# Kernel tuning notes

Measured on AMD Instinct MI355X. Metric: run time of the kernel, lower is better.

Reference implementation:

```python
import jax, jax.numpy as jnp
import numpy as np

B, D, H, O, E, K = 8192, 1024, 4096, 1024, 8, 2

def setup_inputs() -> dict:
    key = jax.random.key(0)
    ks = jax.random.split(key, 8)
    x = jax.random.normal(ks[0], (B, D), dtype=jnp.float32)
    topk_idx = jax.random.randint(ks[1], (B, K), 0, E, dtype=jnp.int32)
    weights = jax.random.uniform(ks[2], (B, K), dtype=jnp.float32)
    s1 = 1.0 / np.sqrt(D)
    s2 = 1.0 / np.sqrt(H)
    W1 = jax.random.uniform(ks[3], (E, D, H), minval=-s1, maxval=s1, dtype=jnp.float32)
    b1 = jax.random.uniform(ks[4], (E, H), minval=-s1, maxval=s1, dtype=jnp.float32)
    W2 = jax.random.uniform(ks[5], (E, H, O), minval=-s2, maxval=s2, dtype=jnp.float32)
    b2 = jax.random.uniform(ks[6], (E, O), minval=-s2, maxval=s2, dtype=jnp.float32)
    return {"x": x, "topk_idx": topk_idx, "weights": weights,
            "W1": W1, "b1": b1, "W2": W2, "b2": b2}

def reference(x, topk_idx, weights, W1, b1, W2, b2):
    # Per-token gate mass for each expert: gate[b,e] = sum_i weights[b,i]*[topk_idx[b,i]==e]
    # Equivalent to the original masked gather/scatter combine (duplicates in topk_idx sum).
    out = jnp.zeros((x.shape[0], W2.shape[-1]), dtype=x.dtype)
    for e in range(W1.shape[0]):  # small fixed loop over experts
        gate_e = jnp.sum(weights * (topk_idx == e), axis=1)  # [B]
        h = jax.nn.relu(x @ W1[e] + b1[e])                   # [B,H]
        out_e = h @ W2[e] + b2[e]                            # [B,O]
        out = out + gate_e[:, None] * out_e
    return out
```

## Files before the change

### kernel.cpp

```cpp
#include <hip/hip_runtime.h>
#include <stdint.h>

#define B_TOK 8192
#define D_DIM 1024
#define H_DIM 4096
#define O_DIM 1024
#define E_NUM 8
#define K_TOP 2
#define NPAIR (B_TOK * K_TOP)

typedef short bf16x8 __attribute__((ext_vector_type(8)));
typedef float f32x4 __attribute__((ext_vector_type(4)));

struct Hdr {
    int counts[8];
    int offsets[9];
    int total1, total2;
    int base1[9];
    int base2[9];
};

__device__ __forceinline__ unsigned short f2bf(float f) {
    union { float f; unsigned int u; } v; v.f = f;
    unsigned int u = v.u;
    unsigned int r = (u + 0x7fffu + ((u >> 16) & 1u)) >> 16;
    return (unsigned short)r;
}

__device__ __forceinline__ float bf2f(unsigned short s) {
    union { unsigned int u; float f; } v;
    v.u = ((unsigned int)s) << 16;
    return v.f;
}

__device__ __forceinline__ void async16(const void* g, const void* l) {
    __builtin_amdgcn_global_load_lds(
        (__attribute__((address_space(1))) void*)(uintptr_t)g,
        (__attribute__((address_space(3))) void*)(uint32_t)(uintptr_t)l,
        16, 0, 0);
}


__global__ void cvt_x_kernel(const float* __restrict__ x, unsigned short* __restrict__ xb) {
    int i = (blockIdx.x * 256 + threadIdx.x) * 4;
    float4 v = *(const float4*)(x + i);
    ushort4 o;
    o.x = f2bf(v.x); o.y = f2bf(v.y); o.z = f2bf(v.z); o.w = f2bf(v.w);
    *(ushort4*)(xb + i) = o;
}

__global__ __launch_bounds__(256) void tconv2_kernel(const float* __restrict__ W1,
                                                     const float* __restrict__ W2,
                                                     unsigned short* __restrict__ o1,
                                                     unsigned short* __restrict__ o2) {
    __shared__ unsigned short tb[64 * 134];
    int z = blockIdx.y;
    int bid = blockIdx.x;
    int R, C;
    const float* ip;
    unsigned short* op;
    if (z < 8) {
        R = D_DIM; C = H_DIM;
        ip = W1 + (size_t)z * R * C;
        op = o1 + (size_t)z * R * C;
    } else {
        R = H_DIM; C = O_DIM;
        ip = W2 + (size_t)(z - 8) * R * C;
        op = o2 + (size_t)(z - 8) * R * C;
    }
    int tR = R >> 7;
    int r0 = (bid % tR) * 128;
    int c0 = (bid / tR) * 64;
    int tid = threadIdx.x;

    int rl = tid >> 4;
    int cg = (tid & 15) * 4;
#pragma unroll
    for (int p = 0; p < 8; p++) {
        int r = rl + p * 16;
        float4 v = *(const float4*)&ip[(size_t)(r0 + r) * C + c0 + cg];
        tb[(cg + 0) * 134 + r] = f2bf(v.x);
        tb[(cg + 1) * 134 + r] = f2bf(v.y);
        tb[(cg + 2) * 134 + r] = f2bf(v.z);
        tb[(cg + 3) * 134 + r] = f2bf(v.w);
    }
    __syncthreads();

    int r16 = (tid & 15) * 8;
#pragma unroll
    for (int i = 0; i < 4; i++) {
        int c = (tid >> 4) + i * 16;
        uint4 v = *(const uint4*)&tb[c * 134 + r16];
        *(uint4*)&op[(size_t)(c0 + c) * R + r0 + r16] = v;
    }
}


__global__ __launch_bounds__(1024) void route_kernel(const int* __restrict__ topk,
                                                     Hdr* hdr,
                                                     int* __restrict__ ptok,
                                                     int* __restrict__ pslot) {
    __shared__ int wcnt[16][8];
    __shared__ int wcur[16][8];
    int tid = threadIdx.x;
    int w = tid >> 6;
    if ((tid & 63) < 8) wcnt[w][tid & 63] = 0;
    __syncthreads();
    int ev[16];
#pragma unroll
    for (int j = 0; j < 16; j++) {
        ev[j] = topk[tid + j * 1024];
        atomicAdd(&wcnt[w][ev[j]], 1);
    }
    __syncthreads();
    if (tid == 0) {
        int off = 0, t1 = 0, t2 = 0;
        for (int e = 0; e < 8; e++) {
            int c = 0;
            for (int w2 = 0; w2 < 16; w2++) {
                wcur[w2][e] = off + c;
                c += wcnt[w2][e];
            }
            hdr->counts[e] = c;
            hdr->offsets[e] = off;
            hdr->base1[e] = t1;
            hdr->base2[e] = t2;
            t1 += ((c + 255) >> 8) * (H_DIM / 256);
            t2 += ((c + 127) >> 7) * (O_DIM / 128);
            off += c;
        }
        hdr->offsets[8] = off;
        hdr->base1[8] = t1;
        hdr->base2[8] = t2;
        hdr->total1 = t1;
        hdr->total2 = t2;
    }
    __syncthreads();
#pragma unroll
    for (int j = 0; j < 16; j++) {
        int i = tid + j * 1024;
        int pos = atomicAdd(&wcur[w][ev[j]], 1);
        ptok[pos] = i >> 1;
        pslot[i] = pos;
    }
}

__global__ void ws_fail_kernel(float* out) { out[0] = 1.0e9f; }


#define ASL(BUF, KH) ((BUF) * 32768 + (KH) * 16384)

#define STG_A(BUF, KH, KOFF) do { \
    async16(Ab + srcA[0] + (KOFF), smem + ASL(BUF, KH) + wu * 2048); \
    async16(Ab + srcA[1] + (KOFF), smem + ASL(BUF, KH) + wu * 2048 + 1024); } while (0)

#define STG_B(BUF, KH, KOFF) do { \
    async16(Bb + srcB[0] + (KOFF), smem + 65536 + ASL(BUF, KH) + wu * 2048); \
    async16(Bb + srcB[1] + (KOFF), smem + 65536 + ASL(BUF, KH) + wu * 2048 + 1024); } while (0)

#define VM6 asm volatile("s_waitcnt vmcnt(6)" ::: "memory")
#define VM0 asm volatile("s_waitcnt vmcnt(0)" ::: "memory")
#define NOPX ((void)0)

#define PHASE0(BUF, KH, STAGE, CKPT) do { \
    STAGE; \
    bq[0] = *(const bf16x8*)&smem[pBo[0] + ASL(BUF, KH)]; \
    bq[1] = *(const bf16x8*)&smem[pBo[1] + ASL(BUF, KH)]; \
    bq[2] = *(const bf16x8*)&smem[pBo[2] + ASL(BUF, KH)]; \
    bq[3] = *(const bf16x8*)&smem[pBo[3] + ASL(BUF, KH)]; \
    aq[0] = *(const bf16x8*)&smem[pAo[0] + ASL(BUF, KH)]; \
    aq[1] = *(const bf16x8*)&smem[pAo[1] + ASL(BUF, KH)]; \
    aq[2] = *(const bf16x8*)&smem[pAo[2] + ASL(BUF, KH)]; \
    aq[3] = *(const bf16x8*)&smem[pAo[3] + ASL(BUF, KH)]; \
    __builtin_amdgcn_s_barrier(); \
    asm volatile("s_waitcnt lgkmcnt(0)" ::: "memory"); \
    __builtin_amdgcn_s_setprio(1); \
    _Pragma("unroll") \
    for (int q_ = 0; q_ < 4; ++q_) { \
        _Pragma("unroll") \
        for (int n_ = 0; n_ < 4; ++n_) \
            acc[q_][n_] = __builtin_amdgcn_mfma_f32_16x16x32_bf16(aq[q_], bq[n_], acc[q_][n_], 0, 0, 0); \
    } \
    __builtin_amdgcn_s_setprio(0); \
    CKPT; \
    __builtin_amdgcn_s_barrier(); \
} while (0)

#define PHASE1(BUF, KH, STAGE, CKPT) do { \
    STAGE; \
    aq[0] = *(const bf16x8*)&smem[pAo[4] + ASL(BUF, KH)]; \
    aq[1] = *(const bf16x8*)&smem[pAo[5] + ASL(BUF, KH)]; \
    aq[2] = *(const bf16x8*)&smem[pAo[6] + ASL(BUF, KH)]; \
    aq[3] = *(const bf16x8*)&smem[pAo[7] + ASL(BUF, KH)]; \
    __builtin_amdgcn_s_barrier(); \
    asm volatile("s_waitcnt lgkmcnt(0)" ::: "memory"); \
    __builtin_amdgcn_s_setprio(1); \
    _Pragma("unroll") \
    for (int q_ = 0; q_ < 4; ++q_) { \
        _Pragma("unroll") \
        for (int n_ = 0; n_ < 4; ++n_) \
            acc[4 + q_][n_] = __builtin_amdgcn_mfma_f32_16x16x32_bf16(aq[q_], bq[n_], acc[4 + q_][n_], 0, 0, 0); \
    } \
    __builtin_amdgcn_s_setprio(0); \
    CKPT; \
    __builtin_amdgcn_s_barrier(); \
} while (0)

template <int KD, int N, bool GATHER>
__global__ __launch_bounds__(512, 2) void moe_gemm256_kernel(
    const unsigned short* __restrict__ A,
    const unsigned short* __restrict__ Bt,
    const float* __restrict__ bias,
    const Hdr* __restrict__ hdr,
    const int* __restrict__ ptok,
    unsigned short* __restrict__ outp,
    int phase) {

    extern __shared__ __align__(16) char smem[];
    constexpr int NT = KD / 64;
    constexpr int NI = NT / 2;
    static_assert(NT >= 4 && (NT % 2) == 0, "K-tile count");

    const int tid = threadIdx.x;
    const int lane = tid & 63;
    const int wv = tid >> 6;
    const int wu = __builtin_amdgcn_readfirstlane(wv);
    const int lr = lane & 15;
    const int lkg = lane >> 4;
    const int wr = wv >> 2;
    const int wc = wv & 3;

    const int total = hdr->total1;
    const int* tb = hdr->base1;

    int chunk = (total + 7) >> 3;
    int seq = (blockIdx.x & 7) * chunk + (blockIdx.x >> 3);
    if (seq >= total) return;

    int e = 0;
#pragma unroll
    for (int j = 1; j < 8; j++)
        if (seq >= tb[j]) e = j;
    e = __builtin_amdgcn_readfirstlane(e);
    int lt = seq - tb[e];
    int cnt = hdr->counts[e], off = hdr->offsets[e];
    int MT = (cnt + 255) >> 8;
    int mtile = lt % MT, ntile = lt / MT;
    if ((ntile >> 3) != phase) return;
    int m0 = mtile * 256, n0 = ntile * 256;

    const char* Ab = (const char*)A;
    const char* Bb = (const char*)(Bt + (size_t)e * ((size_t)N * KD));

    uint32_t srcA[2], srcB[2];
#pragma unroll
    for (int l = 0; l < 2; ++l) {
        int g = wv * 128 + l * 64 + lane;
        int rp = g >> 2, cp = g & 3;
        int c = (cp - (rp >> 1)) & 3;
        int q = off + m0 + rp;
        q = q > NPAIR - 1 ? NPAIR - 1 : q;
        uint32_t rowA = GATHER ? (uint32_t)ptok[q] : (uint32_t)q;
        srcA[l] = rowA * (uint32_t)(KD * 2) + (uint32_t)(c * 16);
        srcB[l] = (uint32_t)(n0 + rp) * (uint32_t)(KD * 2) + (uint32_t)(c * 16);
    }

    uint32_t pAo[8], pBo[4];
#pragma unroll
    for (int mr = 0; mr < 8; ++mr) {
        int r = wr * 128 + mr * 16 + lr;
        pAo[mr] = (uint32_t)(r * 64 + ((lkg + (r >> 1)) & 3) * 16);
    }
#pragma unroll
    for (int nr = 0; nr < 4; ++nr) {
        int r = wc * 64 + nr * 16 + lr;
        pBo[nr] = (uint32_t)(65536 + r * 64 + ((lkg + (r >> 1)) & 3) * 16);
    }

    f32x4 acc[8][4];
#pragma unroll
    for (int i = 0; i < 8; ++i)
#pragma unroll
        for (int j = 0; j < 4; ++j)
            acc[i][j] = (f32x4){0.f, 0.f, 0.f, 0.f};
    bf16x8 aq[4], bq[4];

    STG_A(0, 0, 0u);   STG_B(0, 0, 0u);
    STG_A(0, 1, 64u);  STG_B(0, 1, 64u);
    STG_A(1, 0, 128u); STG_B(1, 0, 128u);
    STG_B(1, 1, 192u);
    VM0;
    __builtin_amdgcn_s_barrier();

    for (int it = 0; it < NI - 1; ++it) {
        const uint32_t kb = (uint32_t)it * 256u;
        PHASE0(0, 0, STG_A(1, 1, kb + 192u), NOPX);
        PHASE1(0, 0, STG_B(0, 0, kb + 256u), NOPX);
        PHASE0(0, 1, STG_A(0, 0, kb + 256u), NOPX);
        PHASE1(0, 1, STG_B(0, 1, kb + 320u), VM6);
        PHASE0(1, 0, STG_A(0, 1, kb + 320u), NOPX);
        PHASE1(1, 0, STG_B(1, 0, kb + 384u), NOPX);
        PHASE0(1, 1, STG_A(1, 0, kb + 384u), NOPX);
        PHASE1(1, 1, STG_B(1, 1, kb + 448u), VM6);
    }
    {
        const uint32_t kb = (uint32_t)(NI - 1) * 256u;
        PHASE0(0, 0, STG_A(1, 1, kb + 192u), NOPX);
        PHASE1(0, 0, NOPX, NOPX);
        PHASE0(0, 1, NOPX, NOPX);
        PHASE1(0, 1, NOPX, VM0);
        PHASE0(1, 0, NOPX, NOPX);
        PHASE1(1, 0, NOPX, NOPX);
        PHASE0(1, 1, NOPX, NOPX);
        PHASE1(1, 1, NOPX, NOPX);
    }

    unsigned short* eb = (unsigned short*)smem;
    int rows_valid = cnt - m0;
    if (rows_valid > 256) rows_valid = 256;
#pragma unroll
    for (int pass = 0; pass < 2; ++pass) {
        __syncthreads();
        if (wr == pass) {
#pragma unroll
            for (int nr = 0; nr < 4; ++nr) {
                int n = wc * 64 + nr * 16 + lr;
                float bv = bias[(size_t)e * N + n0 + n];
#pragma unroll
                for (int mr = 0; mr < 8; ++mr) {
#pragma unroll
                    for (int r2 = 0; r2 < 4; ++r2) {
                        int ml = mr * 16 + lkg * 4 + r2;
                        float v = acc[mr][nr][r2] + bv;
                        if (GATHER) v = v > 0.f ? v : 0.f;
                        eb[ml * 264 + n] = f2bf(v);
                    }
                }
            }
        }
        __syncthreads();
        int rv = rows_valid - pass * 128;
        if (rv > 128) rv = 128;
#pragma unroll
        for (int j = 0; j < 8; ++j) {
            int idx = j * 512 + tid;
            int row = idx >> 5;
            int c16 = idx & 31;
            if (row < rv) {
                uint4 v = *(const uint4*)&eb[row * 264 + c16 * 8];
                *(uint4*)&outp[(size_t)(off + m0 + pass * 128 + row) * N + n0 + c16 * 8] = v;
            }
        }
    }
}

template <int K, int N, bool GATHER>
__global__ __launch_bounds__(256, 4) void moe_gemm128_kernel(
    const unsigned short* __restrict__ A,
    const unsigned short* __restrict__ Bt,
    const float* __restrict__ bias,
    const Hdr* __restrict__ hdr,
    const int* __restrict__ ptok,
    unsigned short* __restrict__ outp,
    int phase) {

    __shared__ __align__(16) unsigned short smem[128 * 132];
    unsigned short* As = smem;
    unsigned short* Bs = smem + 128 * 64;

    const int tid = threadIdx.x;
    const int lane = tid & 63;
    const int wv = tid >> 6;
    const int wu = __builtin_amdgcn_readfirstlane(wv);
    const int wm = (wv & 1) * 64;
    const int wn = (wv >> 1) * 64;
    const int lr = lane & 15;
    const int lkg = lane >> 4;

    const int total = hdr->total2;
    const int* tb = hdr->base2;
    constexpr int NT = N / 128;

    int chunk = (total + 7) >> 3;
    int seq = (blockIdx.x & 7) * chunk + (blockIdx.x >> 3);
    if (seq >= total) return;

    int e = 0;
#pragma unroll
    for (int j = 1; j < 8; j++)
        if (seq >= tb[j]) e = j;
    e = __builtin_amdgcn_readfirstlane(e);
    int lt = seq - tb[e];
    int cnt = hdr->counts[e], off = hdr->offsets[e];
    int MT = (cnt + 127) >> 7;

    int band = lt / (NT * 8);
    int r = lt - band * (NT * 8);
    int mrem = MT - band * 8;
    mrem = mrem > 8 ? 8 : mrem;
    int gsz = mrem * 8;
    int g = r / gsz;
    int rg = r - g * gsz;
    int gm = rg % mrem;
    int gn = rg / mrem;
    int mtile = band * 8 + gm;
    int ntile = g * 8 + gn;
    if ((ntile >> 2) != phase) return;
    int m0 = mtile * 128, n0 = ntile * 128;

    const char* Ab = (const char*)A;
    const char* Bb = (const char*)(Bt + (size_t)e * ((size_t)N * K));
    uint32_t offA[4], offB[4];
#pragma unroll
    for (int i = 0; i < 4; i++) {
        int s = i * 256 + tid;
        int rr = s >> 3;
        int cl = (s & 7) ^ (rr & 7);
        int p = off + m0 + rr;
        p = p > NPAIR - 1 ? NPAIR - 1 : p;
        uint32_t row = GATHER ? (uint32_t)ptok[p] : (uint32_t)p;
        offA[i] = (row * (uint32_t)K + (uint32_t)cl * 8u) * 2u;
        offB[i] = (((uint32_t)(n0 + rr)) * (uint32_t)K + (uint32_t)cl * 8u) * 2u;
    }

    f32x4 zero = {0.f, 0.f, 0.f, 0.f};
    f32x4 acc[4][4];
#pragma unroll
    for (int mt = 0; mt < 4; mt++)
#pragma unroll
        for (int nt = 0; nt < 4; nt++) acc[mt][nt] = zero;

    for (int k0 = 0; k0 < K; k0 += 64) {
#pragma unroll
        for (int i = 0; i < 4; i++) {
            async16(Ab + offA[i], &As[(i * 256 + wu * 64) * 8]);
            async16(Bb + offB[i], &Bs[(i * 256 + wu * 64) * 8]);
            offA[i] += 128;
            offB[i] += 128;
        }
        __syncthreads();
#pragma unroll
        for (int ks = 0; ks < 2; ks++) {
            bf16x8 af[4];
#pragma unroll
            for (int q = 0; q < 4; q++) {
                int ra = wm + q * 16 + lr;
                int ca = (ks * 4 + lkg) ^ (ra & 7);
                af[q] = *(const bf16x8*)&As[ra * 64 + ca * 8];
            }
#pragma unroll
            for (int nt = 0; nt < 4; nt++) {
                int rb = wn + nt * 16 + lr;
                int cb = (ks * 4 + lkg) ^ (rb & 7);
                bf16x8 bfr = *(const bf16x8*)&Bs[rb * 64 + cb * 8];
#pragma unroll
                for (int mt = 0; mt < 4; mt++)
                    acc[mt][nt] = __builtin_amdgcn_mfma_f32_16x16x32_bf16(
                        af[mt], bfr, acc[mt][nt], 0, 0, 0);
            }
        }
        __syncthreads();
    }

#pragma unroll
    for (int nt = 0; nt < 4; nt++) {
        int n = wn + nt * 16 + lr;
        float bv = bias[(size_t)e * N + n0 + n];
#pragma unroll
        for (int mt = 0; mt < 4; mt++) {
#pragma unroll
            for (int r2 = 0; r2 < 4; r2++) {
                int m = wm + mt * 16 + lkg * 4 + r2;
                float v = acc[mt][nt][r2] + bv;
                if (GATHER) v = v > 0.f ? v : 0.f;
                smem[m * 132 + n] = f2bf(v);
            }
        }
    }
    __syncthreads();
    int rows_valid = cnt - m0;
    if (rows_valid > 128) rows_valid = 128;
#pragma unroll
    for (int j = 0; j < 16; j++) {
        int idx = j * 256 + tid;
        int row = idx >> 5;
        int lc8 = idx & 31;
        if (row < rows_valid) {
            uint2 v = *(const uint2*)&smem[row * 132 + lc8 * 4];
            *(uint2*)&outp[(size_t)(off + m0 + row) * N + n0 + lc8 * 4] = v;
        }
    }
}

__global__ void combine_kernel(const unsigned short* __restrict__ oslot,
                               const int* __restrict__ pslot,
                               const float* __restrict__ wts,
                               float* __restrict__ out) {
    int tok = blockIdx.x;
    int s0 = pslot[tok * 2], s1 = pslot[tok * 2 + 1];
    float g0 = wts[tok * 2], g1 = wts[tok * 2 + 1];
    int n = threadIdx.x * 4;
    ushort4 a = *(const ushort4*)&oslot[(size_t)s0 * O_DIM + n];
    ushort4 b = *(const ushort4*)&oslot[(size_t)s1 * O_DIM + n];
    float4 o;
    o.x = g0 * bf2f(a.x) + g1 * bf2f(b.x);
    o.y = g0 * bf2f(a.y) + g1 * bf2f(b.y);
    o.z = g0 * bf2f(a.z) + g1 * bf2f(b.z);
    o.w = g0 * bf2f(a.w) + g1 * bf2f(b.w);
    *(float4*)&out[(size_t)tok * O_DIM + n] = o;
}


extern "C" void kernel_launch(void* const* d_in, const int* in_sizes, int n_in,
                              void* d_out, int out_size, void* d_ws, size_t ws_size,
                              hipStream_t stream) {
    const float* x   = (const float*)d_in[0];
    const int* topk  = (const int*)d_in[1];
    const float* wts = (const float*)d_in[2];
    const float* W1  = (const float*)d_in[3];
    const float* b1  = (const float*)d_in[4];
    const float* W2  = (const float*)d_in[5];
    const float* b2  = (const float*)d_in[6];
    float* out = (float*)d_out;

    char* ws = (char*)d_ws;
    size_t off = 0;
    auto alloc = [&](size_t bytes) -> void* {
        void* p = ws + off;
        off += (bytes + 255) & ~(size_t)255;
        return p;
    };
    Hdr* hdr = (Hdr*)alloc(sizeof(Hdr));
    int* ptok = (int*)alloc((size_t)NPAIR * 4);
    int* pslot = (int*)alloc((size_t)NPAIR * 4);
    unsigned short* xb   = (unsigned short*)alloc((size_t)B_TOK * D_DIM * 2);
    unsigned short* W1bt = (unsigned short*)alloc((size_t)E_NUM * D_DIM * H_DIM * 2);
    unsigned short* W2bt = (unsigned short*)alloc((size_t)E_NUM * H_DIM * O_DIM * 2);
    unsigned short* hbuf = (unsigned short*)alloc((size_t)NPAIR * H_DIM * 2);
    unsigned short* oslot = W1bt;

    if (off > ws_size) {
        hipMemsetAsync(d_out, 0, (size_t)out_size * sizeof(float), stream);
        ws_fail_kernel<<<1, 1, 0, stream>>>(out);
        return;
    }

    static int attr_done = 0;
    if (!attr_done) {
        (void)hipFuncSetAttribute(
            reinterpret_cast<const void*>(&moe_gemm256_kernel<D_DIM, H_DIM, true>),
            hipFuncAttributeMaxDynamicSharedMemorySize, 131072);
        attr_done = 1;
    }

    cvt_x_kernel<<<(B_TOK * D_DIM) / 1024, 256, 0, stream>>>(x, xb);
    tconv2_kernel<<<dim3(512, 16, 1), 256, 0, stream>>>(W1, W2, W1bt, W2bt);
    route_kernel<<<1, 1024, 0, stream>>>(topk, hdr, ptok, pslot);

    moe_gemm256_kernel<D_DIM, H_DIM, true><<<1152, 512, 131072, stream>>>(
        xb, W1bt, b1, hdr, ptok, hbuf, 0);
    moe_gemm256_kernel<D_DIM, H_DIM, true><<<1152, 512, 131072, stream>>>(
        xb, W1bt, b1, hdr, ptok, hbuf, 1);
    moe_gemm128_kernel<H_DIM, O_DIM, false><<<1152, 256, 0, stream>>>(
        hbuf, W2bt, b2, hdr, ptok, oslot, 0);
    moe_gemm128_kernel<H_DIM, O_DIM, false><<<1152, 256, 0, stream>>>(
        hbuf, W2bt, b2, hdr, ptok, oslot, 1);
    combine_kernel<<<B_TOK, 256, 0, stream>>>(oslot, pslot, wts, out);
}
```

Before: 754.1 us.

## Fuse preprocessing kernels and collapse phased GEMM launches into single launches

Merges the x conversion, weight transpose-conversion and routing kernels into one pre_kernel, with block ranges selecting the role and a single 256-thread block doing routing. It also removes the phase split, so each grouped GEMM runs as one launch over all tiles instead of two. The aim is to cut launch gaps and per-launch tail effects. The trade-off is that routing now runs in a 256-thread block that re-reads topk, and the phase split, which may have been there for cache locality of weight tiles, is gone.

```diff
diff --git a/kernel.cpp b/kernel.cpp
--- a/kernel.cpp
+++ b/kernel.cpp
@@ -40,86 +40,85 @@
         16, 0, 0);
 }
 
-
-__global__ void cvt_x_kernel(const float* __restrict__ x, unsigned short* __restrict__ xb) {
-    int i = (blockIdx.x * 256 + threadIdx.x) * 4;
-    float4 v = *(const float4*)(x + i);
-    ushort4 o;
-    o.x = f2bf(v.x); o.y = f2bf(v.y); o.z = f2bf(v.z); o.w = f2bf(v.w);
-    *(ushort4*)(xb + i) = o;
-}
-
-__global__ __launch_bounds__(256) void tconv2_kernel(const float* __restrict__ W1,
-                                                     const float* __restrict__ W2,
-                                                     unsigned short* __restrict__ o1,
-                                                     unsigned short* __restrict__ o2) {
+__global__ __launch_bounds__(256) void pre_kernel(
+    const float* __restrict__ x, unsigned short* __restrict__ xb,
+    const float* __restrict__ W1, const float* __restrict__ W2,
+    unsigned short* __restrict__ o1, unsigned short* __restrict__ o2,
+    const int* __restrict__ topk, Hdr* __restrict__ hdr,
+    int* __restrict__ ptok, int* __restrict__ pslot) {
+
     __shared__ unsigned short tb[64 * 134];
-    int z = blockIdx.y;
     int bid = blockIdx.x;
-    int R, C;
-    const float* ip;
-    unsigned short* op;
-    if (z < 8) {
-        R = D_DIM; C = H_DIM;
-        ip = W1 + (size_t)z * R * C;
-        op = o1 + (size_t)z * R * C;
-    } else {
-        R = H_DIM; C = O_DIM;
-        ip = W2 + (size_t)(z - 8) * R * C;
-        op = o2 + (size_t)(z - 8) * R * C;
-    }
-    int tR = R >> 7;
-    int r0 = (bid % tR) * 128;
-    int c0 = (bid / tR) * 64;
     int tid = threadIdx.x;
 
-    int rl = tid >> 4;
-    int cg = (tid & 15) * 4;
-#pragma unroll
-    for (int p = 0; p < 8; p++) {
-        int r = rl + p * 16;
-        float4 v = *(const float4*)&ip[(size_t)(r0 + r) * C + c0 + cg];
-        tb[(cg + 0) * 134 + r] = f2bf(v.x);
-        tb[(cg + 1) * 134 + r] = f2bf(v.y);
-        tb[(cg + 2) * 134 + r] = f2bf(v.z);
-        tb[(cg + 3) * 134 + r] = f2bf(v.w);
-    }
+    if (bid < 8192) {
+        int i = (bid * 256 + tid) * 4;
+        float4 v = *(const float4*)(x + i);
+        ushort4 o;
+        o.x = f2bf(v.x); o.y = f2bf(v.y); o.z = f2bf(v.z); o.w = f2bf(v.w);
+        *(ushort4*)(xb + i) = o;
+        return;
+    }
+
+    if (bid < 16384) {
+        int bt = bid - 8192;
+        int z = bt >> 9;
+        int sub = bt & 511;
+        int R, C;
+        const float* ip;
+        unsigned short* op;
+        if (z < 8) {
+            R = D_DIM; C = H_DIM;
+            ip = W1 + (size_t)z * R * C;
+            op = o1 + (size_t)z * R * C;
+        } else {
+            R = H_DIM; C = O_DIM;
+            ip = W2 + (size_t)(z - 8) * R * C;
+            op = o2 + (size_t)(z - 8) * R * C;
+        }
+        int tR = R >> 7;
+        int r0 = (sub % tR) * 128;
+        int c0 = (sub / tR) * 64;
+
+        int rl = tid >> 4;
+        int cg = (tid & 15) * 4;
+#pragma unroll
+        for (int p = 0; p < 8; p++) {
+            int r = rl + p * 16;
+            float4 v = *(const float4*)&ip[(size_t)(r0 + r) * C + c0 + cg];
+            tb[(cg + 0) * 134 + r] = f2bf(v.x);
+            tb[(cg + 1) * 134 + r] = f2bf(v.y);
+            tb[(cg + 2) * 134 + r] = f2bf(v.z);
+            tb[(cg + 3) * 134 + r] = f2bf(v.w);
+        }
+        __syncthreads();
+        int r16 = (tid & 15) * 8;
+#pragma unroll
+        for (int i = 0; i < 4; i++) {
+            int c = (tid >> 4) + i * 16;
+            uint4 v = *(const uint4*)&tb[c * 134 + r16];
+            *(uint4*)&op[(size_t)(c0 + c) * R + r0 + r16] = v;
+        }
+        return;
+    }
+
+    int* wcnt = (int*)tb;
+    int* wcur = wcnt + 32;
+    int w = tid >> 6;
+    if ((tid & 63) < 8) wcnt[w * 8 + (tid & 63)] = 0;
     __syncthreads();
-
-    int r16 = (tid & 15) * 8;
-#pragma unroll
-    for (int i = 0; i < 4; i++) {
-        int c = (tid >> 4) + i * 16;
-        uint4 v = *(const uint4*)&tb[c * 134 + r16];
-        *(uint4*)&op[(size_t)(c0 + c) * R + r0 + r16] = v;
-    }
-}
-
-
-__global__ __launch_bounds__(1024) void route_kernel(const int* __restrict__ topk,
-                                                     Hdr* hdr,
-                                                     int* __restrict__ ptok,
-                                                     int* __restrict__ pslot) {
-    __shared__ int wcnt[16][8];
-    __shared__ int wcur[16][8];
-    int tid = threadIdx.x;
-    int w = tid >> 6;
-    if ((tid & 63) < 8) wcnt[w][tid & 63] = 0;
-    __syncthreads();
-    int ev[16];
-#pragma unroll
-    for (int j = 0; j < 16; j++) {
-        ev[j] = topk[tid + j * 1024];
-        atomicAdd(&wcnt[w][ev[j]], 1);
+    for (int j = 0; j < 64; j++) {
+        int e = topk[tid + j * 256];
+        atomicAdd(&wcnt[w * 8 + e], 1);
     }
     __syncthreads();
     if (tid == 0) {
         int off = 0, t1 = 0, t2 = 0;
         for (int e = 0; e < 8; e++) {
             int c = 0;
-            for (int w2 = 0; w2 < 16; w2++) {
-                wcur[w2][e] = off + c;
-                c += wcnt[w2][e];
+            for (int w2 = 0; w2 < 4; w2++) {
+                wcur[w2 * 8 + e] = off + c;
+                c += wcnt[w2 * 8 + e];
             }
             hdr->counts[e] = c;
             hdr->offsets[e] = off;
@@ -136,10 +135,10 @@
         hdr->total2 = t2;
     }
     __syncthreads();
-#pragma unroll
-    for (int j = 0; j < 16; j++) {
-        int i = tid + j * 1024;
-        int pos = atomicAdd(&wcur[w][ev[j]], 1);
+    for (int j = 0; j < 64; j++) {
+        int i = tid + j * 256;
+        int e = topk[i];
+        int pos = atomicAdd(&wcur[w * 8 + e], 1);
         ptok[pos] = i >> 1;
         pslot[i] = pos;
     }
@@ -213,8 +212,7 @@
     const float* __restrict__ bias,
     const Hdr* __restrict__ hdr,
     const int* __restrict__ ptok,
-    unsigned short* __restrict__ outp,
-    int phase) {
+    unsigned short* __restrict__ outp) {
 
     extern __shared__ __align__(16) char smem[];
     constexpr int NT = KD / 64;
@@ -246,7 +244,6 @@
     int cnt = hdr->counts[e], off = hdr->offsets[e];
     int MT = (cnt + 255) >> 8;
     int mtile = lt % MT, ntile = lt / MT;
-    if ((ntile >> 3) != phase) return;
     int m0 = mtile * 256, n0 = ntile * 256;
 
     const char* Ab = (const char*)A;
@@ -361,8 +358,7 @@
     const float* __restrict__ bias,
     const Hdr* __restrict__ hdr,
     const int* __restrict__ ptok,
-    unsigned short* __restrict__ outp,
-    int phase) {
+    unsigned short* __restrict__ outp) {
 
     __shared__ __align__(16) unsigned short smem[128 * 132];
     unsigned short* As = smem;
@@ -405,7 +401,6 @@
     int gn = rg / mrem;
     int mtile = band * 8 + gm;
     int ntile = g * 8 + gn;
-    if ((ntile >> 2) != phase) return;
     int m0 = mtile * 128, n0 = ntile * 128;
 
     const char* Ab = (const char*)A;
@@ -553,17 +548,12 @@
         attr_done = 1;
     }
 
-    cvt_x_kernel<<<(B_TOK * D_DIM) / 1024, 256, 0, stream>>>(x, xb);
-    tconv2_kernel<<<dim3(512, 16, 1), 256, 0, stream>>>(W1, W2, W1bt, W2bt);
-    route_kernel<<<1, 1024, 0, stream>>>(topk, hdr, ptok, pslot);
+    pre_kernel<<<16385, 256, 0, stream>>>(x, xb, W1, W2, W1bt, W2bt,
+                                          topk, hdr, ptok, pslot);
 
     moe_gemm256_kernel<D_DIM, H_DIM, true><<<1152, 512, 131072, stream>>>(
-        xb, W1bt, b1, hdr, ptok, hbuf, 0);
-    moe_gemm256_kernel<D_DIM, H_DIM, true><<<1152, 512, 131072, stream>>>(
-        xb, W1bt, b1, hdr, ptok, hbuf, 1);
+        xb, W1bt, b1, hdr, ptok, hbuf);
     moe_gemm128_kernel<H_DIM, O_DIM, false><<<1152, 256, 0, stream>>>(
-        hbuf, W2bt, b2, hdr, ptok, oslot, 0);
-    moe_gemm128_kernel<H_DIM, O_DIM, false><<<1152, 256, 0, stream>>>(
-        hbuf, W2bt, b2, hdr, ptok, oslot, 1);
+        hbuf, W2bt, b2, hdr, ptok, oslot);
     combine_kernel<<<B_TOK, 256, 0, stream>>>(oslot, pslot, wts, out);
 }
```

Result: faster. 722.6 us (-4.2%).
